# Performance work log

Hardware: AMD Instinct MI355X
Metric: run time of the kernel (lower is better)

Reference implementation:

```python
import jax, jax.numpy as jnp
import numpy as np

N_HEAD = 16


def setup_inputs() -> dict:
    key = jax.random.key(0)
    k1, k2, k3 = jax.random.split(key, 3)
    B, T, C = 4, 2048, 2048
    x = jax.random.normal(k1, (B, T, C), dtype=jnp.float32)
    # GPT-style small init so attention logits are in a sane range
    W_attn = jax.random.normal(k2, (3 * C, C), dtype=jnp.float32) * 0.02
    W_proj = jax.random.normal(k3, (C, C), dtype=jnp.float32) * 0.02
    return {"x": x, "W_attn": W_attn, "W_proj": W_proj}


def reference(x, W_attn, W_proj):
    B, T, C = x.shape
    H = N_HEAD
    d = C // H
    # c_attn: eqx.nn.Linear(weight [3C, C]) applied per-token -> x @ W_attn.T
    qkv = jnp.einsum('btc,fc->btf', x, W_attn)  # [B, T, 3C]
    q, k, v = jnp.split(qkv, 3, axis=-1)
    q = q.reshape(B, T, H, d).transpose(0, 2, 1, 3)  # [B, H, T, d]
    k = k.reshape(B, T, H, d).transpose(0, 2, 1, 3)
    v = v.reshape(B, T, H, d).transpose(0, 2, 1, 3)
    att = jnp.einsum('bhqd,bhkd->bhqk', q, k)  # [B, H, T, T]
    # causal mask: positions j > i are masked (future tokens)
    causal = jnp.tril(jnp.ones((T, T), dtype=bool))
    att = jnp.where(causal, att, -jnp.inf)
    att = jax.nn.softmax(att / jnp.sqrt(jnp.asarray(d, att.dtype)), axis=-1)
    out = jnp.einsum('bhqk,bhkd->bhqd', att, v)  # [B, H, T, d]
    out = out.transpose(0, 2, 1, 3).reshape(B, T, C)
    # c_proj -> out @ W_proj.T
    return jnp.einsum('btc,oc->bto', out, W_proj)
```

## Files before the change

kernel.cpp:

```cpp
#include <hip/hip_runtime.h>
#include <hip/hip_bf16.h>
#include <stdint.h>

typedef __hip_bfloat16 bf16;
typedef __attribute__((ext_vector_type(8))) __bf16 bf16x8;
typedef __attribute__((ext_vector_type(8))) unsigned short ushort8;
typedef __attribute__((ext_vector_type(4))) float floatx4;

#define MFMA_16x16x32(a, b, c) __builtin_amdgcn_mfma_f32_16x16x32_bf16((a), (b), (c), 0, 0, 0)

__device__ __forceinline__ void async_load16(const bf16* g, bf16* l) {
  __builtin_amdgcn_global_load_lds(
      (const __attribute__((address_space(1))) unsigned int*)g,
      (__attribute__((address_space(3))) unsigned int*)l,
      16, 0, 0);
}

template <int CTRL>
__device__ __forceinline__ float dpp_f(float x) {
  return __builtin_bit_cast(float, __builtin_amdgcn_update_dpp(
      0, __builtin_bit_cast(int, x), CTRL, 0xf, 0xf, true));
}
__device__ __forceinline__ float row_max16(float x) {
  x = fmaxf(x, dpp_f<0xB1>(x));
  x = fmaxf(x, dpp_f<0x4E>(x));
  x = fmaxf(x, dpp_f<0x124>(x));
  x = fmaxf(x, dpp_f<0x128>(x));
  return x;
}
__device__ __forceinline__ float row_sum16(float x) {
  x += dpp_f<0xB1>(x);
  x += dpp_f<0x4E>(x);
  x += dpp_f<0x124>(x);
  x += dpp_f<0x128>(x);
  return x;
}

__global__ __launch_bounds__(256)
void f32_to_bf16_k(const float* __restrict__ in, bf16* __restrict__ out, int n)
{
  const int i = (blockIdx.x * 256 + threadIdx.x) * 8;
  if (i >= n) return;
  bf16 tmp[8];
#pragma unroll
  for (int j = 0; j < 8; ++j) tmp[j] = __float2bfloat16(in[i + j]);
  *(ushort8*)&out[i] = *(const ushort8*)tmp;
}

#define G_BAR __builtin_amdgcn_s_barrier()

#define G_STAGE(pg, ls, tt, h)                                                  \
  do {                                                                          \
    async_load16((pg) + (size_t)((h) * 64) * K + (size_t)(tt) * 64,             \
                 (ls) + (h) * 4096 + lws);                                      \
    async_load16((pg) + (size_t)((h) * 64 + 128) * K + (size_t)(tt) * 64,       \
                 (ls) + (h) * 4096 + 8192 + lws);                               \
  } while (0)

#define G_RD_A(mh)                                                              \
  _Pragma("unroll") for (int i = 0; i < 4; ++i) {                               \
    const int rb = (wm * 128 + (mh) * 64 + i * 16 + l16) * 64;                  \
    af[i][0] = *(const bf16x8*)&sAd[rb + ach0];                                 \
    af[i][1] = *(const bf16x8*)&sAd[rb + ach1];                                 \
  }

#define G_RD_B(dst, nh)                                                         \
  _Pragma("unroll") for (int j = 0; j < 2; ++j) {                               \
    const int rb = (wn * 64 + (nh) * 32 + j * 16 + l16) * 64;                   \
    dst[j][0] = *(const bf16x8*)&sBd[rb + ach0];                                \
    dst[j][1] = *(const bf16x8*)&sBd[rb + ach1];                                \
  }

#define G_MM(mh, nh, BF)                                                        \
  __builtin_amdgcn_s_setprio(1);                                                \
  _Pragma("unroll") for (int kk = 0; kk < 2; ++kk)                              \
  _Pragma("unroll") for (int i = 0; i < 4; ++i)                                 \
  _Pragma("unroll") for (int j = 0; j < 2; ++j)                                 \
    acc[(mh) * 4 + i][(nh) * 2 + j] =                                           \
        MFMA_16x16x32(af[i][kk], BF[j][kk], acc[(mh) * 4 + i][(nh) * 2 + j]);   \
  __builtin_amdgcn_s_setprio(0);

__global__ __launch_bounds__(512, 2)
void gemm_bt(const bf16* __restrict__ A, const bf16* __restrict__ B,
             bf16* __restrict__ Cb, float* __restrict__ Cf,
             int M, int N, int K)
{
  __shared__ __align__(16) bf16 sA[2][256 * 64];
  __shared__ __align__(16) bf16 sB[2][256 * 64];

  const int tid  = threadIdx.x;
  const int lane = tid & 63;
  const int w    = tid >> 6;
  const int wm   = w >> 2;
  const int wn   = w & 3;
  const int quad = lane >> 4;
  const int l16  = lane & 15;

  const int nbx = N >> 8;
  const int nwg = nbx * (M >> 8);
  const int wg  = (blockIdx.x & 7) * (nwg >> 3) + (blockIdx.x >> 3);
  const int tileM = (wg / nbx) << 8;
  const int tileN = (wg % nbx) << 8;

  const int srow = tid >> 3;
  const int scol = ((tid & 7) ^ (srow & 7)) << 3;
  const bf16* pA = A + (size_t)(tileM + srow) * K + scol;
  const bf16* pB = B + (size_t)(tileN + srow) * K + scol;
  const int lws = w * 512;

  const int ach0 = ((quad ^ (l16 & 7)) << 3);
  const int ach1 = (((4 + quad) ^ (l16 & 7)) << 3);

  floatx4 acc[8][4];
#pragma unroll
  for (int i = 0; i < 8; ++i)
#pragma unroll
    for (int j = 0; j < 4; ++j) acc[i][j] = (floatx4){0.f, 0.f, 0.f, 0.f};

  const int T = K >> 6;

  G_STAGE(pA, &sA[0][0], 0, 0);
  G_STAGE(pB, &sB[0][0], 0, 0);
  G_STAGE(pB, &sB[0][0], 0, 1);
  G_STAGE(pA, &sA[0][0], 0, 1);
  if (T > 1) {
    G_STAGE(pA, &sA[1][0], 1, 0);
    G_STAGE(pB, &sB[1][0], 1, 0);
    asm volatile("s_waitcnt vmcnt(4)" ::: "memory");
  } else {
    asm volatile("s_waitcnt vmcnt(0)" ::: "memory");
  }
  G_BAR;

  bf16x8 af[4][2], bf0[2][2], bf1[2][2];
  for (int t = 0; t < T; ++t) {
    const bf16* sAd = &sA[t & 1][0];
    const bf16* sBd = &sB[t & 1][0];
    bf16* sAn = &sA[(t + 1) & 1][0];
    bf16* sBn = &sB[(t + 1) & 1][0];
    bf16* sAc = &sA[t & 1][0];
    bf16* sBc = &sB[t & 1][0];

    G_RD_A(0); G_RD_B(bf0, 0);
    if (t + 1 < T) G_STAGE(pB, sBn, t + 1, 1);
    G_BAR; G_MM(0, 0, bf0); G_BAR;

    G_RD_B(bf1, 1);
    if (t + 1 < T) G_STAGE(pA, sAn, t + 1, 1);
    G_BAR; G_MM(0, 1, bf1); G_BAR;

    G_RD_A(1);
    if (t + 2 < T) G_STAGE(pA, sAc, t + 2, 0);
    G_BAR; G_MM(1, 0, bf0); G_BAR;

    if (t + 2 < T) G_STAGE(pB, sBc, t + 2, 0);
    G_BAR; G_MM(1, 1, bf1);
    if (t + 2 < T) asm volatile("s_waitcnt vmcnt(4)" ::: "memory");
    else           asm volatile("s_waitcnt vmcnt(0)" ::: "memory");
    G_BAR;
  }

  const int orow = tileM + wm * 128 + quad * 4;
  const int ocol = tileN + wn * 64 + l16;
  if (Cf) {
#pragma unroll
    for (int fm = 0; fm < 8; ++fm)
#pragma unroll
      for (int fn = 0; fn < 4; ++fn)
#pragma unroll
        for (int r = 0; r < 4; ++r)
          Cf[(size_t)(orow + fm * 16 + r) * N + ocol + fn * 16] = acc[fm][fn][r];
  } else {
#pragma unroll
    for (int fm = 0; fm < 8; ++fm)
#pragma unroll
      for (int fn = 0; fn < 4; ++fn)
#pragma unroll
        for (int r = 0; r < 4; ++r)
          Cb[(size_t)(orow + fm * 16 + r) * N + ocol + fn * 16] =
              __float2bfloat16(acc[fm][fn][r]);
  }
}

__global__ __launch_bounds__(256)
void transpose_v(const bf16* __restrict__ qkv, bf16* __restrict__ Vt)
{
  __shared__ bf16 tile[64 * 128];
  const int t0 = blockIdx.x * 64;
  const int bh = blockIdx.y;
  const int b = bh >> 4;
  const int h = bh & 15;
  const int tid = threadIdx.x;
  const bf16* src = qkv + (size_t)(b * 2048 + t0) * 6144 + 4096 + h * 128;
#pragma unroll
  for (int s = 0; s < 4; ++s) {
    const int cid = s * 256 + tid;
    const int row = cid >> 4;
    const int col = (cid & 15) << 3;
    *(ushort8*)&tile[row * 128 + col] = *(const ushort8*)&src[(size_t)row * 6144 + col];
  }
  __syncthreads();
  const int dim = tid >> 1;
  const int tp  = (tid & 1) << 5;
  bf16 vals[32];
#pragma unroll
  for (int t = 0; t < 32; ++t) vals[t] = tile[(tp + t) * 128 + dim];
  bf16* dst = Vt + (size_t)(bh * 128 + dim) * 2048 + t0 + tp;
#pragma unroll
  for (int s = 0; s < 4; ++s) *(ushort8*)&dst[s * 8] = ((const ushort8*)vals)[s];
}

__global__ __launch_bounds__(256, 2)
void flash_attn(const bf16* __restrict__ qkv, const bf16* __restrict__ Vt,
                bf16* __restrict__ outb)
{
  __shared__ __align__(16) bf16 smem[16384 + 4 * 32 * 40];
  bf16* sP = smem + 16384;

  const int qb  = gridDim.y - 1 - blockIdx.y;
  const int bh  = blockIdx.x;
  const int b   = bh >> 4;
  const int h   = bh & 15;
  const int tid = threadIdx.x;
  const int lane = tid & 63;
  const int w    = tid >> 6;
  const int quad = lane >> 4;
  const int l16  = lane & 15;

  const size_t rs = 6144;
  const bf16* Qg = qkv + (size_t)(b * 2048 + qb * 128) * rs + h * 128;
  const bf16* Kg = qkv + (size_t)(b * 2048) * rs + 2048 + h * 128;
  const bf16* Vg = Vt + (size_t)bh * 128 * 2048;

#pragma unroll
  for (int s = 0; s < 8; ++s) {
    const int cid = (w * 8 + s) * 64 + lane;
    const int row = cid >> 4;
    const int col = ((cid & 15) ^ (row & 15)) << 3;
    async_load16(Qg + (size_t)row * rs + col, &smem[(w * 8 + s) * 512]);
  }
  __syncthreads();

  bf16x8 qf[2][4];
#pragma unroll
  for (int i = 0; i < 2; ++i)
#pragma unroll
    for (int kc = 0; kc < 4; ++kc)
      qf[i][kc] = *(const bf16x8*)&smem[(w * 32 + i * 16 + l16) * 128 + (((kc * 4 + quad) ^ l16) << 3)];
  __syncthreads();

  int kq_row[2], kq_col[2], vv_row[2], vv_col[2];
#pragma unroll
  for (int s = 0; s < 2; ++s) {
    const int cid = (w * 2 + s) * 64 + lane;
    kq_row[s] = cid >> 4;
    kq_col[s] = ((cid & 15) ^ (kq_row[s] & 15)) << 3;
    vv_row[s] = cid >> 2;
    vv_col[s] = ((cid & 3) ^ (vv_row[s] & 3)) << 3;
  }

  const int kb_end = 4 * qb + 4;
#pragma unroll
  for (int s = 0; s < 2; ++s) {
    async_load16(Kg + (size_t)kq_row[s] * rs + kq_col[s],      &smem[(w * 2 + s) * 512]);
    async_load16(Vg + (size_t)vv_row[s] * 2048 + vv_col[s],    &smem[4096 + (w * 2 + s) * 512]);
  }

  floatx4 o[2][8];
#pragma unroll
  for (int i = 0; i < 2; ++i)
#pragma unroll
    for (int s = 0; s < 8; ++s) o[i][s] = (floatx4){0.f, 0.f, 0.f, 0.f};
  float m_i[2][4], l_i[2][4];
#pragma unroll
  for (int i = 0; i < 2; ++i)
#pragma unroll
    for (int r = 0; r < 4; ++r) { m_i[i][r] = -__builtin_inff(); l_i[i][r] = 0.f; }

  const float csc = 1.4426950408889634f * 0.08838834764831845f;

  for (int kb = 0; kb < kb_end; ++kb) {
    __syncthreads();
    if (kb + 1 < kb_end) {
      bf16* nb = smem + ((kb + 1) & 1) * 8192;
#pragma unroll
      for (int s = 0; s < 2; ++s) {
        async_load16(Kg + (size_t)((kb + 1) * 32 + kq_row[s]) * rs + kq_col[s], nb + (w * 2 + s) * 512);
        async_load16(Vg + (size_t)vv_row[s] * 2048 + (kb + 1) * 32 + vv_col[s], nb + 4096 + (w * 2 + s) * 512);
      }
    }
    if (kb * 32 > qb * 128 + w * 32 + 31) continue;

    const bf16* sK = smem + (kb & 1) * 8192;
    const bf16* sV = sK + 4096;

    floatx4 sacc[2][2];
#pragma unroll
    for (int i = 0; i < 2; ++i)
#pragma unroll
      for (int j = 0; j < 2; ++j) sacc[i][j] = (floatx4){0.f, 0.f, 0.f, 0.f};
#pragma unroll
    for (int kc = 0; kc < 4; ++kc) {
      const int ch = ((kc * 4 + quad) ^ l16) << 3;
#pragma unroll
      for (int j = 0; j < 2; ++j) {
        const bf16x8 bk = *(const bf16x8*)&sK[(j * 16 + l16) * 128 + ch];
        sacc[0][j] = MFMA_16x16x32(qf[0][kc], bk, sacc[0][j]);
        sacc[1][j] = MFMA_16x16x32(qf[1][kc], bk, sacc[1][j]);
      }
    }

    const bool diag = (kb * 32 + 31 > qb * 128 + w * 32);
    float p[2][2][4];
#pragma unroll
    for (int i = 0; i < 2; ++i) {
      const int qrow = qb * 128 + w * 32 + i * 16 + quad * 4;
#pragma unroll
      for (int r = 0; r < 4; ++r) {
        float mx = -__builtin_inff();
#pragma unroll
        for (int j = 0; j < 2; ++j) {
          float v = sacc[i][j][r] * csc;
          if (diag && kb * 32 + j * 16 + l16 > qrow + r) v = -__builtin_inff();
          p[i][j][r] = v;
          mx = fmaxf(mx, v);
        }
        mx = row_max16(mx);
        const float mnew = fmaxf(m_i[i][r], mx);
        const float alpha = __builtin_amdgcn_exp2f(m_i[i][r] - mnew);
        m_i[i][r] = mnew;
        float rsl = 0.f;
#pragma unroll
        for (int j = 0; j < 2; ++j) {
          const float e = __builtin_amdgcn_exp2f(p[i][j][r] - mnew);
          p[i][j][r] = e;
          rsl += e;
        }
        l_i[i][r] = alpha * l_i[i][r] + row_sum16(rsl);
#pragma unroll
        for (int s = 0; s < 8; ++s) o[i][s][r] *= alpha;
      }
    }

#pragma unroll
    for (int i = 0; i < 2; ++i)
#pragma unroll
      for (int j = 0; j < 2; ++j)
#pragma unroll
        for (int r = 0; r < 4; ++r)
          sP[w * 1280 + (i * 16 + quad * 4 + r) * 40 + j * 16 + l16] = __float2bfloat16(p[i][j][r]);

    const bf16x8 ap0 = *(const bf16x8*)&sP[w * 1280 + l16 * 40 + quad * 8];
    const bf16x8 ap1 = *(const bf16x8*)&sP[w * 1280 + (16 + l16) * 40 + quad * 8];
    const int chv = (quad ^ (l16 & 3)) << 3;
#pragma unroll
    for (int s = 0; s < 8; ++s) {
      const bf16x8 bv = *(const bf16x8*)&sV[(s * 16 + l16) * 32 + chv];
      o[0][s] = MFMA_16x16x32(ap0, bv, o[0][s]);
      o[1][s] = MFMA_16x16x32(ap1, bv, o[1][s]);
    }
  }

#pragma unroll
  for (int i = 0; i < 2; ++i) {
    float rl[4];
#pragma unroll
    for (int r = 0; r < 4; ++r) rl[r] = 1.f / l_i[i][r];
    bf16* dst = outb + (size_t)(b * 2048 + qb * 128 + w * 32 + i * 16) * 2048 + h * 128;
#pragma unroll
    for (int s = 0; s < 8; ++s)
#pragma unroll
      for (int r = 0; r < 4; ++r)
        dst[(size_t)(quad * 4 + r) * 2048 + s * 16 + l16] = __float2bfloat16(o[i][s][r] * rl[r]);
  }
}

extern "C" void kernel_launch(void* const* d_in, const int* in_sizes, int n_in,
                              void* d_out, int out_size, void* d_ws, size_t ws_size,
                              hipStream_t stream)
{
  (void)in_sizes; (void)n_in; (void)out_size; (void)ws_size;
  const float* x  = (const float*)d_in[0];
  const float* Wa = (const float*)d_in[1];
  const float* Wp = (const float*)d_in[2];
  float* out = (float*)d_out;
  char* ws = (char*)d_ws;

  bf16* xb   = (bf16*)(ws + 0);
  bf16* Wab  = (bf16*)(ws + 33554432ull);
  bf16* Wpb  = (bf16*)(ws + 58720256ull);
  bf16* qkv  = (bf16*)(ws + 67108864ull);
  bf16* attb = (bf16*)(ws + 167772160ull);
  bf16* Vt   = xb;

  f32_to_bf16_k<<<8192, 256, 0, stream>>>(x,  xb,  4 * 2048 * 2048);
  f32_to_bf16_k<<<6144, 256, 0, stream>>>(Wa, Wab, 3 * 2048 * 2048);
  f32_to_bf16_k<<<2048, 256, 0, stream>>>(Wp, Wpb, 2048 * 2048);

  gemm_bt<<<dim3(768), 512, 0, stream>>>(xb, Wab, qkv, nullptr, 8192, 6144, 2048);
  transpose_v<<<dim3(32, 64), 256, 0, stream>>>(qkv, Vt);
  flash_attn<<<dim3(64, 16), 256, 0, stream>>>(qkv, Vt, attb);
  gemm_bt<<<dim3(256), 512, 0, stream>>>(attb, Wpb, nullptr, out, 8192, 2048, 2048);
}
```

Measured before the change: 577.0 us.

## Restructure GEMM main loop with double-buffered A fragments and fewer barriers

Reworks the software pipeline of the bf16 GEMM kernel. It now keeps two A-fragment register sets so the next tile's first A half is read from LDS during the current tile's MFMAs. The loop drops from eight barriers per K-step to four, and global-to-LDS staging and vmcnt waits are reordered. The aim is to cut barrier stalls and overlap LDS reads and async loads with matrix math. In exchange it uses more registers, and the hand-counted vmcnt values risk races if they are wrong.

Result: slower. 609.6 us (+5.6%).

```diff
diff --git a/kernel.cpp b/kernel.cpp
--- a/kernel.cpp
+++ b/kernel.cpp
@@ -49,35 +49,47 @@
 
 #define G_BAR __builtin_amdgcn_s_barrier()
 
-#define G_STAGE(pg, ls, tt, h)                                                  \
+#define ST_A(buf, tt, h)                                                        \
   do {                                                                          \
-    async_load16((pg) + (size_t)((h) * 64) * K + (size_t)(tt) * 64,             \
-                 (ls) + (h) * 4096 + lws);                                      \
-    async_load16((pg) + (size_t)((h) * 64 + 128) * K + (size_t)(tt) * 64,       \
-                 (ls) + (h) * 4096 + 8192 + lws);                               \
+    async_load16(pA + (size_t)((h) * 64) * K + (size_t)(tt) * 64,               \
+                 &sA[buf][(h) * 4096 + lws]);                                   \
+    async_load16(pA + (size_t)((h) * 64 + 128) * K + (size_t)(tt) * 64,         \
+                 &sA[buf][(h) * 4096 + 8192 + lws]);                            \
   } while (0)
 
-#define G_RD_A(mh)                                                              \
-  _Pragma("unroll") for (int i = 0; i < 4; ++i) {                               \
-    const int rb = (wm * 128 + (mh) * 64 + i * 16 + l16) * 64;                  \
-    af[i][0] = *(const bf16x8*)&sAd[rb + ach0];                                 \
-    af[i][1] = *(const bf16x8*)&sAd[rb + ach1];                                 \
-  }
-
-#define G_RD_B(dst, nh)                                                         \
-  _Pragma("unroll") for (int j = 0; j < 2; ++j) {                               \
-    const int rb = (wn * 64 + (nh) * 32 + j * 16 + l16) * 64;                   \
-    dst[j][0] = *(const bf16x8*)&sBd[rb + ach0];                                \
-    dst[j][1] = *(const bf16x8*)&sBd[rb + ach1];                                \
-  }
-
-#define G_MM(mh, nh, BF)                                                        \
+#define ST_B(buf, tt, h)                                                        \
+  do {                                                                          \
+    async_load16(pB + (size_t)((h) * 64) * K + (size_t)(tt) * 64,               \
+                 &sB[buf][(h) * 4096 + lws]);                                   \
+    async_load16(pB + (size_t)((h) * 64 + 128) * K + (size_t)(tt) * 64,         \
+                 &sB[buf][(h) * 4096 + 8192 + lws]);                            \
+  } while (0)
+
+#define RD_A(dst, sAd, mh)                                                      \
+  do {                                                                          \
+    _Pragma("unroll") for (int i = 0; i < 4; ++i) {                             \
+      const int rb = (wm * 128 + (mh) * 64 + i * 16 + l16) * 64;                \
+      dst[i][0] = *(const bf16x8*)&(sAd)[rb + ach0];                            \
+      dst[i][1] = *(const bf16x8*)&(sAd)[rb + ach1];                            \
+    }                                                                           \
+  } while (0)
+
+#define RD_B(dst, sBd, nh)                                                      \
+  do {                                                                          \
+    _Pragma("unroll") for (int j = 0; j < 2; ++j) {                             \
+      const int rb = (wn * 64 + (nh) * 32 + j * 16 + l16) * 64;                 \
+      dst[j][0] = *(const bf16x8*)&(sBd)[rb + ach0];                            \
+      dst[j][1] = *(const bf16x8*)&(sBd)[rb + ach1];                            \
+    }                                                                           \
+  } while (0)
+
+#define G_MM(mh, nh, AF, BF)                                                    \
   __builtin_amdgcn_s_setprio(1);                                                \
   _Pragma("unroll") for (int kk = 0; kk < 2; ++kk)                              \
   _Pragma("unroll") for (int i = 0; i < 4; ++i)                                 \
   _Pragma("unroll") for (int j = 0; j < 2; ++j)                                 \
     acc[(mh) * 4 + i][(nh) * 2 + j] =                                           \
-        MFMA_16x16x32(af[i][kk], BF[j][kk], acc[(mh) * 4 + i][(nh) * 2 + j]);   \
+        MFMA_16x16x32(AF[i][kk], BF[j][kk], acc[(mh) * 4 + i][(nh) * 2 + j]);   \
   __builtin_amdgcn_s_setprio(0);
 
 __global__ __launch_bounds__(512, 2)
@@ -119,45 +131,43 @@
 
   const int T = K >> 6;
 
-  G_STAGE(pA, &sA[0][0], 0, 0);
-  G_STAGE(pB, &sB[0][0], 0, 0);
-  G_STAGE(pB, &sB[0][0], 0, 1);
-  G_STAGE(pA, &sA[0][0], 0, 1);
-  if (T > 1) {
-    G_STAGE(pA, &sA[1][0], 1, 0);
-    G_STAGE(pB, &sB[1][0], 1, 0);
-    asm volatile("s_waitcnt vmcnt(4)" ::: "memory");
-  } else {
-    asm volatile("s_waitcnt vmcnt(0)" ::: "memory");
-  }
+  bf16x8 af0[4][2], af1[4][2], bf0[2][2], bf1[2][2];
+
+  ST_A(0, 0, 0); ST_B(0, 0, 0); ST_A(0, 0, 1); ST_B(0, 0, 1);
+  ST_A(1, 1, 0); ST_B(1, 1, 0); ST_A(1, 1, 1); ST_B(1, 1, 1);
+  asm volatile("s_waitcnt vmcnt(14)" ::: "memory");
   G_BAR;
-
-  bf16x8 af[4][2], bf0[2][2], bf1[2][2];
+  RD_A(af0, (&sA[0][0]), 0);
+
   for (int t = 0; t < T; ++t) {
-    const bf16* sAd = &sA[t & 1][0];
-    const bf16* sBd = &sB[t & 1][0];
-    bf16* sAn = &sA[(t + 1) & 1][0];
-    bf16* sBn = &sB[(t + 1) & 1][0];
-    bf16* sAc = &sA[t & 1][0];
-    bf16* sBc = &sB[t & 1][0];
-
-    G_RD_A(0); G_RD_B(bf0, 0);
-    if (t + 1 < T) G_STAGE(pB, sBn, t + 1, 1);
-    G_BAR; G_MM(0, 0, bf0); G_BAR;
-
-    G_RD_B(bf1, 1);
-    if (t + 1 < T) G_STAGE(pA, sAn, t + 1, 1);
-    G_BAR; G_MM(0, 1, bf1); G_BAR;
-
-    G_RD_A(1);
-    if (t + 2 < T) G_STAGE(pA, sAc, t + 2, 0);
-    G_BAR; G_MM(1, 0, bf0); G_BAR;
-
-    if (t + 2 < T) G_STAGE(pB, sBc, t + 2, 0);
-    G_BAR; G_MM(1, 1, bf1);
-    if (t + 2 < T) asm volatile("s_waitcnt vmcnt(4)" ::: "memory");
-    else           asm volatile("s_waitcnt vmcnt(0)" ::: "memory");
+    const int P = t & 1;
+    const bf16* sAd = &sA[P][0];
+    const bf16* sBd = &sB[P][0];
+    const bf16* sAn = &sA[P ^ 1][0];
+
+    if (t + 1 < T) { asm volatile("s_waitcnt vmcnt(8)" ::: "memory"); }
+    else           { asm volatile("s_waitcnt vmcnt(0)" ::: "memory"); }
     G_BAR;
+    RD_B(bf0, sBd, 0);
+    RD_B(bf1, sBd, 1);
+    if (t + 2 < T) { ST_A(P, t + 2, 0); }
+    G_MM(0, 0, af0, bf0);
+
+    G_BAR;
+    RD_A(af1, sAd, 1);
+    G_MM(0, 1, af0, bf1);
+
+    if (t + 2 < T)      { asm volatile("s_waitcnt vmcnt(8)" ::: "memory"); }
+    else if (t + 1 < T) { asm volatile("s_waitcnt vmcnt(6)" ::: "memory"); }
+    else                { asm volatile("s_waitcnt vmcnt(0)" ::: "memory"); }
+    G_BAR;
+    if (t + 1 < T) { RD_A(af0, sAn, 0); }
+    if (t + 2 < T) { ST_B(P, t + 2, 0); }
+    G_MM(1, 1, af1, bf1);
+
+    G_BAR;
+    if (t + 2 < T) { ST_A(P, t + 2, 1); ST_B(P, t + 2, 1); }
+    G_MM(1, 0, af1, bf0);
   }
 
   const int orow = tileM + wm * 128 + quad * 4;
```
